# Optimization experiments

Hardware: AMD Instinct MI355X
Metric: run time of the kernel (lower is better)

## Reference

```python
import jax, jax.numpy as jnp
import numpy as np

BS, C, H, W = 4, 128, 64, 64  # input_dim=128
INNER = 64


def setup_inputs() -> dict:
    key = jax.random.key(0)
    ks = jax.random.split(key, 9)
    s_in = 1.0 / np.sqrt(C)
    s_inner = 1.0 / np.sqrt(INNER)
    return {
        "inpt": jax.random.normal(ks[0], (BS, C, H, W), dtype=jnp.float32),
        "Wq": jax.random.normal(ks[1], (INNER, C), dtype=jnp.float32) * s_in,
        "bq": jax.random.normal(ks[2], (INNER,), dtype=jnp.float32) * 0.01,
        "Wk": jax.random.normal(ks[3], (INNER, C), dtype=jnp.float32) * s_in,
        "bk": jax.random.normal(ks[4], (INNER,), dtype=jnp.float32) * 0.01,
        "Wv": jax.random.normal(ks[5], (INNER, C), dtype=jnp.float32) * s_in,
        "bv": jax.random.normal(ks[6], (INNER,), dtype=jnp.float32) * 0.01,
        "Wo": jax.random.normal(ks[7], (C, INNER), dtype=jnp.float32) * s_inner,
        "bo": jax.random.normal(ks[8], (C,), dtype=jnp.float32) * 0.01,
    }


def reference(inpt, Wq, bq, Wk, bk, Wv, bv, Wo, bo):
    bs, c, h, w = inpt.shape
    L = h * w
    # [bs, C, H, W] -> [bs, L, C] (tokens = spatial positions)
    x = inpt.reshape(bs, c, L).transpose(0, 2, 1)
    q = jnp.einsum('blc,dc->bld', x, Wq) + bq  # [bs, L, INNER]
    k = jnp.einsum('blc,dc->bld', x, Wk) + bk
    v = jnp.einsum('blc,dc->bld', x, Wv) + bv
    # torch code divides by np.round(sqrt(d), 2); for d=64 this is exactly 8.0
    scale = jnp.float32(np.round(np.sqrt(q.shape[-1]), 2))
    scores = jnp.einsum('bld,bmd->blm', q, k) / scale  # [bs, L, L] score matrix
    factors = jax.nn.softmax(scores, axis=-1)
    ctx = jnp.einsum('blm,bmd->bld', factors, v)  # [bs, L, INNER]
    out = jnp.einsum('bld,cd->blc', ctx, Wo) + bo  # [bs, L, C]
    out = out.transpose(0, 2, 1).reshape(bs, c, h, w)
    return inpt + out
```

## Files before the change

kernel.cpp:

```cpp
#include <hip/hip_runtime.h>
#include <hip/hip_bf16.h>

typedef __bf16 bf16x8 __attribute__((ext_vector_type(8)));
typedef __bf16 bf16x4 __attribute__((ext_vector_type(4)));
typedef short  s16x4  __attribute__((ext_vector_type(4)));
typedef float  f32x4  __attribute__((ext_vector_type(4)));

#define MFMA32(a, b, c) __builtin_amdgcn_mfma_f32_16x16x32_bf16((a), (b), (c), 0, 0, 0)
#define MFMA16K(a, b, c) __builtin_amdgcn_mfma_f32_16x16x16bf16_1k((a), (b), (c), 0, 0, 0)

#if __has_builtin(__builtin_amdgcn_exp2f)
#define EXP2F(x) __builtin_amdgcn_exp2f(x)
#else
#define EXP2F(x) __expf(0.6931471805599453f * (x))
#endif

#define GL16(G, L)                                                            \
    __builtin_amdgcn_global_load_lds(                                         \
        (const __attribute__((address_space(1))) void*)(G),                   \
        (__attribute__((address_space(3))) void*)(L), 16, 0, 0)

#define SPLIT 4
#define QSCALE 0.18033688011112042f
#define BBOUND 12.0f

__global__ __launch_bounds__(256) void qkv_kernel(
    const float* __restrict__ inpt,
    const float* __restrict__ Wq, const float* __restrict__ bq,
    const float* __restrict__ Wk, const float* __restrict__ bk,
    const float* __restrict__ Wv, const float* __restrict__ bv,
    __bf16* __restrict__ Qws, __bf16* __restrict__ Kws, __bf16* __restrict__ VTws)
{
    __shared__ __align__(16) __bf16 xT[16 * 140];
    __shared__ __align__(16) __bf16 os[16 * 144];
    const int bid = blockIdx.x;
    const int b   = bid >> 8;
    const int l0  = (bid & 255) << 4;
    const int t   = threadIdx.x;

    {
        const int c = t >> 1, half = t & 1;
        const float* xin = inpt + ((size_t)(b * 128 + c)) * 4096 + l0 + half * 8;
        float4 v0 = *(const float4*)xin;
        float4 v1 = *(const float4*)(xin + 4);
        const int tok0 = half * 8;
        xT[(tok0 + 0) * 140 + c] = (__bf16)v0.x;
        xT[(tok0 + 1) * 140 + c] = (__bf16)v0.y;
        xT[(tok0 + 2) * 140 + c] = (__bf16)v0.z;
        xT[(tok0 + 3) * 140 + c] = (__bf16)v0.w;
        xT[(tok0 + 4) * 140 + c] = (__bf16)v1.x;
        xT[(tok0 + 5) * 140 + c] = (__bf16)v1.y;
        xT[(tok0 + 6) * 140 + c] = (__bf16)v1.z;
        xT[(tok0 + 7) * 140 + c] = (__bf16)v1.w;
    }
    __syncthreads();

    const int w    = t >> 6;
    const int lane = t & 63;
    const int quad = lane >> 4;
    const int l15  = lane & 15;

    f32x4 acc[3];
    #pragma unroll
    for (int j = 0; j < 3; ++j)
        #pragma unroll
        for (int r = 0; r < 4; ++r) acc[j][r] = 0.f;

    #pragma unroll
    for (int ks = 0; ks < 4; ++ks) {
        bf16x8 af = *(const bf16x8*)&xT[l15 * 140 + ks * 32 + quad * 8];
        #pragma unroll
        for (int j = 0; j < 3; ++j) {
            const int wn   = w * 3 + j;
            const int msel = wn >> 2;
            const float* W = (msel == 0) ? Wq : ((msel == 1) ? Wk : Wv);
            const float* Wp = W + ((wn & 3) * 16 + l15) * 128 + ks * 32 + quad * 8;
            float4 wa = *(const float4*)Wp;
            float4 wb = *(const float4*)(Wp + 4);
            bf16x8 bf;
            bf[0] = (__bf16)wa.x; bf[1] = (__bf16)wa.y;
            bf[2] = (__bf16)wa.z; bf[3] = (__bf16)wa.w;
            bf[4] = (__bf16)wb.x; bf[5] = (__bf16)wb.y;
            bf[6] = (__bf16)wb.z; bf[7] = (__bf16)wb.w;
            acc[j] = MFMA32(af, bf, acc[j]);
        }
    }

    #pragma unroll
    for (int j = 0; j < 3; ++j) {
        const int wn   = w * 3 + j;
        const int msel = wn >> 2;
        const int o0   = (wn & 3) * 16;
        const float* bb = (msel == 0) ? bq : ((msel == 1) ? bk : bv);
        float bias = bb[o0 + l15];
        if (msel < 2) {
            const float scl = (msel == 0) ? QSCALE : 1.0f;
            const int oc = wn * 16 + l15;
            #pragma unroll
            for (int r = 0; r < 4; ++r)
                os[(quad * 4 + r) * 144 + oc] = (__bf16)((acc[j][r] + bias) * scl);
        } else {
            const int d = o0 + l15;
            bf16x4 v;
            #pragma unroll
            for (int r = 0; r < 4; ++r) v[r] = (__bf16)(acc[j][r] + bias);
            *(bf16x4*)(VTws + ((size_t)(b * 64 + d)) * 4096 + l0 + quad * 4) = v;
        }
    }
    __syncthreads();

    {
        const int tok = t >> 4, c = t & 15;
        bf16x8 v = *(const bf16x8*)&os[tok * 144 + c * 8];
        __bf16* dst = (c < 8)
            ? Qws + ((size_t)(b * 4096 + l0 + tok)) * 64 + c * 8
            : Kws + ((size_t)(b * 4096 + l0 + tok)) * 64 + (c - 8) * 8;
        *(bf16x8*)dst = v;
    }
}

__global__ __launch_bounds__(256, 4) void attn_kernel(
    const __bf16* __restrict__ Qws, const __bf16* __restrict__ Kws,
    const __bf16* __restrict__ VTws,
    float* __restrict__ Ops, float* __restrict__ Lws)
{
    __shared__ __align__(16) __bf16 sbuf[2][8192];

    const int bid   = blockIdx.x;
    const int split = bid >> 8;
    const int qt    = bid & 255;
    const int b  = qt >> 6;
    const int l0 = (qt & 63) << 6;
    const int t    = threadIdx.x;
    const int w    = t >> 6;
    const int lane = t & 63;
    const int quad = lane >> 4;
    const int l15  = lane & 15;
    const int l7   = l15 & 7;

    const __bf16* qptr = Qws + ((size_t)(b * 4096 + l0 + w * 16 + l15)) * 64 + quad * 8;
    bf16x8 qf0 = *(const bf16x8*)qptr;
    bf16x8 qf1 = *(const bf16x8*)(qptr + 32);

    f32x4 cfr[4];
    #pragma unroll
    for (int mt = 0; mt < 4; ++mt)
        #pragma unroll
        for (int r = 0; r < 4; ++r) cfr[mt][r] = 0.f;
    float l_run = 0.f;

    const uint4* Kg = (const uint4*)(Kws + ((size_t)b << 18));
    const uint4* Vg = (const uint4*)(VTws + ((size_t)b << 18));
    const int rw = t >> 3, cw = (t & 7) ^ ((t >> 3) & 7);
    const uint4* kp = Kg + rw * 8 + cw + split * 8192;
    const uint4* vp = Vg + (size_t)rw * 512 + cw + split * 128;

    union B4 { bf16x4 h; s16x4 s; };

    {
        __bf16* Bb = sbuf[0];
        GL16(kp,         Bb +        w * 512);
        GL16(kp + 256,   Bb + 2048 + w * 512);
        GL16(vp,         Bb + 4096 + w * 512);
        GL16(vp + 16384, Bb + 6144 + w * 512);
        kp += 512; vp += 8;
    }

    for (int kt = 0; kt < 16; ++kt) {
        const int cur = kt & 1;
        __syncthreads();
        if (kt < 15) {
            __bf16* Bb = sbuf[cur ^ 1];
            GL16(kp,         Bb +        w * 512);
            GL16(kp + 256,   Bb + 2048 + w * 512);
            GL16(vp,         Bb + 4096 + w * 512);
            GL16(vp + 16384, Bb + 6144 + w * 512);
            kp += 512; vp += 8;
        }
        const __bf16* B = sbuf[cur];

        float psum = 0.f;
        B4 pk[4];
        #pragma unroll
        for (int nt = 0; nt < 4; ++nt) {
            const int key = nt * 16 + l15;
            const int sw  = key * 8;
            const int kx  = key & 7;
            bf16x8 kf0 = *(const bf16x8*)&B[(sw + (quad ^ kx)) * 8];
            bf16x8 kf1 = *(const bf16x8*)&B[(sw + ((quad + 4) ^ kx)) * 8];
            f32x4 a = {-BBOUND, -BBOUND, -BBOUND, -BBOUND};
            a = MFMA32(kf0, qf0, a);
            a = MFMA32(kf1, qf1, a);
            #pragma unroll
            for (int r = 0; r < 4; ++r) {
                float p = EXP2F(a[r]);
                psum += p;
                pk[nt].h[r] = (__bf16)p;
            }
        }
        psum += __shfl_xor(psum, 16);
        psum += __shfl_xor(psum, 32);
        l_run += psum;

        const __bf16* Vb = B + 4096;
        const int q2 = quad >> 1, q1 = (quad & 1) * 4;
        #pragma unroll
        for (int kc = 0; kc < 4; ++kc) {
            #pragma unroll
            for (int mt = 0; mt < 4; ++mt) {
                const int d  = mt * 16 + l15;
                const int cc = (2 * kc + q2) ^ l7;
                B4 vf;
                vf.h = *(const bf16x4*)&Vb[(d * 8 + cc) * 8 + q1];
                cfr[mt] = MFMA16K(vf.s, pk[kc].s, cfr[mt]);
            }
        }
    }

    const int l   = l0 + w * 16 + l15;
    const int row = (split * 4 + b) * 4096 + l;
    float* obase = Ops + (size_t)row * 64;
    #pragma unroll
    for (int mt = 0; mt < 4; ++mt)
        *(f32x4*)(obase + mt * 16 + quad * 4) = cfr[mt];
    if (quad == 0) Lws[row] = l_run;
}

__global__ __launch_bounds__(256) void outproj_kernel(
    const float* __restrict__ inpt,
    const float* __restrict__ Ops, const float* __restrict__ Lws,
    const float* __restrict__ Wo, const float* __restrict__ bo,
    float* __restrict__ out)
{
    __shared__ __align__(16) __bf16 cx[16 * 72];
    const int bid = blockIdx.x;
    const int b   = bid >> 8;
    const int l0  = (bid & 255) << 4;
    const int t   = threadIdx.x;

    {
        const int token = t >> 4, d4 = (t & 15) << 2;
        const int rowb  = b * 4096 + l0 + token;
        float denom = 0.f;
        #pragma unroll
        for (int s = 0; s < SPLIT; ++s) denom += Lws[s * 16384 + rowb];
        const float inv = 1.f / denom;
        float ax = 0.f, ay = 0.f, az = 0.f, aw = 0.f;
        #pragma unroll
        for (int s = 0; s < SPLIT; ++s) {
            const float4 v = *(const float4*)(Ops + ((size_t)(s * 16384 + rowb)) * 64 + d4);
            ax += v.x; ay += v.y; az += v.z; aw += v.w;
        }
        bf16x4 pv;
        pv[0] = (__bf16)(ax * inv); pv[1] = (__bf16)(ay * inv);
        pv[2] = (__bf16)(az * inv); pv[3] = (__bf16)(aw * inv);
        *(bf16x4*)&cx[token * 72 + d4] = pv;
    }
    __syncthreads();

    const int w    = t >> 6;
    const int lane = t & 63;
    const int quad = lane >> 4;
    const int l15  = lane & 15;

    f32x4 acc[2];
    #pragma unroll
    for (int mi = 0; mi < 2; ++mi)
        #pragma unroll
        for (int r = 0; r < 4; ++r) acc[mi][r] = 0.f;

    #pragma unroll
    for (int ks = 0; ks < 2; ++ks) {
        bf16x8 bfrag = *(const bf16x8*)&cx[l15 * 72 + ks * 32 + quad * 8];
        #pragma unroll
        for (int mi = 0; mi < 2; ++mi) {
            const int crow = (w * 2 + mi) * 16 + l15;
            const float* Wp = Wo + crow * 64 + ks * 32 + quad * 8;
            float4 wa = *(const float4*)Wp;
            float4 wb = *(const float4*)(Wp + 4);
            bf16x8 afrag;
            afrag[0] = (__bf16)wa.x; afrag[1] = (__bf16)wa.y;
            afrag[2] = (__bf16)wa.z; afrag[3] = (__bf16)wa.w;
            afrag[4] = (__bf16)wb.x; afrag[5] = (__bf16)wb.y;
            afrag[6] = (__bf16)wb.z; afrag[7] = (__bf16)wb.w;
            acc[mi] = MFMA32(afrag, bfrag, acc[mi]);
        }
    }

    #pragma unroll
    for (int mi = 0; mi < 2; ++mi) {
        #pragma unroll
        for (int r = 0; r < 4; ++r) {
            const int c = (w * 2 + mi) * 16 + quad * 4 + r;
            const size_t addr = ((size_t)(b * 128 + c)) * 4096 + l0 + l15;
            out[addr] = inpt[addr] + bo[c] + acc[mi][r];
        }
    }
}

extern "C" void kernel_launch(void* const* d_in, const int* in_sizes, int n_in,
                              void* d_out, int out_size, void* d_ws, size_t ws_size,
                              hipStream_t stream)
{
    const float* inpt = (const float*)d_in[0];
    const float* Wq   = (const float*)d_in[1];
    const float* bq   = (const float*)d_in[2];
    const float* Wk   = (const float*)d_in[3];
    const float* bk   = (const float*)d_in[4];
    const float* Wv   = (const float*)d_in[5];
    const float* bv   = (const float*)d_in[6];
    const float* Wo   = (const float*)d_in[7];
    const float* bo   = (const float*)d_in[8];
    float* out = (float*)d_out;

    char* ws = (char*)d_ws;
    const size_t MB = (size_t)1 << 20;
    __bf16* Qws  = (__bf16*)(ws + 0 * MB);
    __bf16* Kws  = (__bf16*)(ws + 2 * MB);
    __bf16* VTws = (__bf16*)(ws + 4 * MB);
    float*  Ops  = (float*)(ws + 6 * MB);
    float*  Lws  = (float*)(ws + 23 * MB);

    qkv_kernel<<<1024, 256, 0, stream>>>(inpt, Wq, bq, Wk, bk, Wv, bv, Qws, Kws, VTws);
    attn_kernel<<<SPLIT * 256, 256, 0, stream>>>(Qws, Kws, VTws, Ops, Lws);
    outproj_kernel<<<1024, 256, 0, stream>>>(inpt, Ops, Lws, Wo, bo, out);
}
```

Baseline: 127.8 us.

## Tile V^T per key block so attention loads 16-byte V fragments

The QKV kernel now writes V^T in a per-64-key-tile layout (d rows by 64 keys, grouped by k-chunk), so the attention kernel stages V with the same contiguous pattern as K. It reads one 16-byte V fragment feeding two MFMAs instead of two 8-byte reads. LDS offsets are precomputed once into register arrays, and the main loop is unrolled by two with fixed buffer pointers. The exp partial sums are also tree-reduced. The cost is higher register pressure from the offset arrays and an additional layout coupling between the two kernels.

```diff
diff --git a/kernel.cpp b/kernel.cpp
--- a/kernel.cpp
+++ b/kernel.cpp
@@ -23,6 +23,7 @@
 #define SPLIT 4
 #define QSCALE 0.18033688011112042f
 #define BBOUND 12.0f
+
 
 __global__ __launch_bounds__(256) void qkv_kernel(
     const float* __restrict__ inpt,
@@ -100,11 +101,14 @@
             for (int r = 0; r < 4; ++r)
                 os[(quad * 4 + r) * 144 + oc] = (__bf16)((acc[j][r] + bias) * scl);
         } else {
-            const int d = o0 + l15;
+            const int d  = o0 + l15;
+            const int kt = l0 >> 6;
+            const int kc = (l0 >> 4) & 3;
             bf16x4 v;
             #pragma unroll
             for (int r = 0; r < 4; ++r) v[r] = (__bf16)(acc[j][r] + bias);
-            *(bf16x4*)(VTws + ((size_t)(b * 64 + d)) * 4096 + l0 + quad * 4) = v;
+            *(bf16x4*)(VTws + (size_t)b * 262144 + kt * 4096
+                       + d * 64 + quad * 16 + kc * 4) = v;
         }
     }
     __syncthreads();
@@ -136,7 +140,6 @@
     const int lane = t & 63;
     const int quad = lane >> 4;
     const int l15  = lane & 15;
-    const int l7   = l15 & 7;
 
     const __bf16* qptr = Qws + ((size_t)(b * 4096 + l0 + w * 16 + l15)) * 64 + quad * 8;
     bf16x8 qf0 = *(const bf16x8*)qptr;
@@ -148,73 +151,84 @@
         #pragma unroll
         for (int r = 0; r < 4; ++r) cfr[mt][r] = 0.f;
     float l_run = 0.f;
+
+    int koff[8], voff[8];
+    #pragma unroll
+    for (int nt = 0; nt < 4; ++nt) {
+        const int key = nt * 16 + l15;
+        const int kx  = key & 7;
+        koff[nt * 2 + 0] = (key * 8 + (quad ^ kx)) * 8;
+        koff[nt * 2 + 1] = (key * 8 + ((quad + 4) ^ kx)) * 8;
+    }
+    #pragma unroll
+    for (int mt = 0; mt < 4; ++mt) {
+        const int d = mt * 16 + l15;
+        #pragma unroll
+        for (int kc8 = 0; kc8 < 2; ++kc8)
+            voff[kc8 * 4 + mt] = 4096 + d * 64 + (((2 * quad + kc8) ^ (d & 7)) * 8);
+    }
 
     const uint4* Kg = (const uint4*)(Kws + ((size_t)b << 18));
     const uint4* Vg = (const uint4*)(VTws + ((size_t)b << 18));
     const int rw = t >> 3, cw = (t & 7) ^ ((t >> 3) & 7);
     const uint4* kp = Kg + rw * 8 + cw + split * 8192;
-    const uint4* vp = Vg + (size_t)rw * 512 + cw + split * 128;
+    const uint4* vp = Vg + rw * 8 + cw + split * 8192;
 
     union B4 { bf16x4 h; s16x4 s; };
-
-    {
-        __bf16* Bb = sbuf[0];
-        GL16(kp,         Bb +        w * 512);
-        GL16(kp + 256,   Bb + 2048 + w * 512);
-        GL16(vp,         Bb + 4096 + w * 512);
-        GL16(vp + 16384, Bb + 6144 + w * 512);
-        kp += 512; vp += 8;
-    }
-
-    for (int kt = 0; kt < 16; ++kt) {
-        const int cur = kt & 1;
-        __syncthreads();
-        if (kt < 15) {
-            __bf16* Bb = sbuf[cur ^ 1];
-            GL16(kp,         Bb +        w * 512);
-            GL16(kp + 256,   Bb + 2048 + w * 512);
-            GL16(vp,         Bb + 4096 + w * 512);
-            GL16(vp + 16384, Bb + 6144 + w * 512);
-            kp += 512; vp += 8;
-        }
-        const __bf16* B = sbuf[cur];
-
-        float psum = 0.f;
+    union V8 { bf16x8 v; s16x4 q[2]; };
+
+    auto stage = [&](__bf16* Bb) {
+        GL16(kp,       Bb +        w * 512);
+        GL16(kp + 256, Bb + 2048 + w * 512);
+        GL16(vp,       Bb + 4096 + w * 512);
+        GL16(vp + 256, Bb + 6144 + w * 512);
+        kp += 512; vp += 512;
+    };
+
+    auto tile_step = [&](const __bf16* __restrict__ B) {
         B4 pk[4];
+        float ps[4];
         #pragma unroll
         for (int nt = 0; nt < 4; ++nt) {
-            const int key = nt * 16 + l15;
-            const int sw  = key * 8;
-            const int kx  = key & 7;
-            bf16x8 kf0 = *(const bf16x8*)&B[(sw + (quad ^ kx)) * 8];
-            bf16x8 kf1 = *(const bf16x8*)&B[(sw + ((quad + 4) ^ kx)) * 8];
+            bf16x8 kf0 = *(const bf16x8*)&B[koff[nt * 2 + 0]];
+            bf16x8 kf1 = *(const bf16x8*)&B[koff[nt * 2 + 1]];
             f32x4 a = {-BBOUND, -BBOUND, -BBOUND, -BBOUND};
             a = MFMA32(kf0, qf0, a);
             a = MFMA32(kf1, qf1, a);
-            #pragma unroll
-            for (int r = 0; r < 4; ++r) {
-                float p = EXP2F(a[r]);
-                psum += p;
-                pk[nt].h[r] = (__bf16)p;
-            }
-        }
+            float p0 = EXP2F(a[0]), p1 = EXP2F(a[1]);
+            float p2 = EXP2F(a[2]), p3 = EXP2F(a[3]);
+            pk[nt].h[0] = (__bf16)p0; pk[nt].h[1] = (__bf16)p1;
+            pk[nt].h[2] = (__bf16)p2; pk[nt].h[3] = (__bf16)p3;
+            ps[nt] = (p0 + p1) + (p2 + p3);
+        }
+        float psum = (ps[0] + ps[1]) + (ps[2] + ps[3]);
         psum += __shfl_xor(psum, 16);
         psum += __shfl_xor(psum, 32);
         l_run += psum;
 
-        const __bf16* Vb = B + 4096;
-        const int q2 = quad >> 1, q1 = (quad & 1) * 4;
-        #pragma unroll
-        for (int kc = 0; kc < 4; ++kc) {
+        #pragma unroll
+        for (int kc8 = 0; kc8 < 2; ++kc8) {
             #pragma unroll
             for (int mt = 0; mt < 4; ++mt) {
-                const int d  = mt * 16 + l15;
-                const int cc = (2 * kc + q2) ^ l7;
-                B4 vf;
-                vf.h = *(const bf16x4*)&Vb[(d * 8 + cc) * 8 + q1];
-                cfr[mt] = MFMA16K(vf.s, pk[kc].s, cfr[mt]);
+                V8 vv;
+                vv.v = *(const bf16x8*)&B[voff[kc8 * 4 + mt]];
+                cfr[mt] = MFMA16K(vv.q[0], pk[2 * kc8 + 0].s, cfr[mt]);
+                cfr[mt] = MFMA16K(vv.q[1], pk[2 * kc8 + 1].s, cfr[mt]);
             }
         }
+    };
+
+    stage(sbuf[0]);
+
+    __bf16* B0 = sbuf[0];
+    __bf16* B1 = sbuf[1];
+    for (int kt2 = 0; kt2 < 8; ++kt2) {
+        __syncthreads();
+        stage(B1);
+        tile_step(B0);
+        __syncthreads();
+        if (kt2 < 7) stage(B0);
+        tile_step(B1);
     }
 
     const int l   = l0 + w * 16 + l15;
```

Measured after the change: 125.9 us. About the same (-1.4%).
